# Optimization experiments

Measured on AMD Instinct MI355X. Metric: run time of the kernel, lower is better.

## Reference

```python
import jax, jax.numpy as jnp
import numpy as np

B, S, I, F = 2048, 512, 256, 256  # batch, seq_length, input_size, filter_num


def setup_inputs() -> dict:
    key = jax.random.key(0)
    ks = jax.random.split(key, 9)
    sc = 0.05
    return {
        "hidden": jax.random.normal(ks[0], (B, I), jnp.float32),
        "inp": jax.random.normal(ks[1], (B, S, I), jnp.float32),
        "W1": jax.random.normal(ks[2], (F, I), jnp.float32) * sc,   # linear1 weight (no bias)
        "Wc": jax.random.normal(ks[3], (F, S), jnp.float32) * sc,   # conv kernel [F,1,S,1] squeezed
        "bc": jax.random.normal(ks[4], (F,), jnp.float32) * sc,     # conv bias
        "W2": jax.random.normal(ks[5], (I, I + F), jnp.float32) * sc,
        "b2": jax.random.normal(ks[6], (I,), jnp.float32) * sc,
        "Wfc": jax.random.normal(ks[7], (1, I), jnp.float32) * sc,
        "bfc": jax.random.normal(ks[8], (1,), jnp.float32) * sc,
    }


def reference(hidden, inp, W1, Wc, bc, W2, b2, Wfc, bfc):
    # w = linear1(hidden).unsqueeze(1): [B,1,F]
    w = hidden @ W1.T  # [B,F]
    # Conv2d(1,F,kernel=(S,1)) over input [B,1,S,I] -> [B,F,1,I]; kernel spans full
    # time axis with width 1, so it's a contraction over t per input channel i.
    Hc_raw = jnp.einsum('bti,ft->bfi', inp, Wc) + bc[None, :, None]  # [B,F,I]
    # faithful to torch: .squeeze().reshape([-1, input_size, filter_num])
    H_c = Hc_raw.reshape(-1, I, F)  # [B,I,F]
    s = jnp.sum(H_c * w[:, None, :], axis=2)          # [B,I]
    a = jax.nn.sigmoid(s)
    v = jnp.sum(a[:, :, None] * H_c, axis=1)          # [B,F]
    concat = jnp.concatenate([hidden, v], axis=1)     # [B,I+F]
    h_prime = concat @ W2.T + b2                      # [B,I]
    out = h_prime @ Wfc.T + bfc                       # [B,1]
    return out
```

## Files before the change

kernel.cpp:

```cpp
#include <hip/hip_runtime.h>

#define B_ 2048
#define S_ 512
#define I_ 256
#define F_ 256
#define NG 8

#define OFF_W    0
#define OFF_SW   (OFF_W + B_*F_)
#define OFF_U    (OFF_SW + B_)
#define OFF_P    (OFF_U + B_*S_)
#define OFF_RP   (OFF_P + B_*S_)

__global__ __launch_bounds__(256) void k_pre(
    const float* __restrict__ hidden, const float* __restrict__ W1,
    const float* __restrict__ W2, const float* __restrict__ Wfc,
    float* __restrict__ ws) {
  const int tid = threadIdx.x;

  if (blockIdx.x >= B_ / 4) {
    const int g = blockIdx.x - B_ / 4;
    float acc0 = 0.f, acc1 = 0.f;
#pragma unroll 8
    for (int ii = 0; ii < 32; ++ii) {
      const int i = g * 32 + ii;
      const float f = Wfc[i];
      acc0 += f * W2[(size_t)i * (I_ + F_) + tid];
      acc1 += f * W2[(size_t)i * (I_ + F_) + tid + 256];
    }
    ws[OFF_RP + g * 512 + tid] = acc0;
    ws[OFF_RP + g * 512 + 256 + tid] = acc1;
    return;
  }

  __shared__ float h[4][I_];
  __shared__ float red[256];
  const int b0 = blockIdx.x * 4;
#pragma unroll
  for (int k = 0; k < 4; ++k) h[k][tid] = hidden[(size_t)(b0 + k) * I_ + tid];
  __syncthreads();

  const int f = tid;
  const float4* wrow = (const float4*)(W1 + (size_t)f * I_);
  float acc[4] = {0.f, 0.f, 0.f, 0.f};
#pragma unroll 4
  for (int iq = 0; iq < I_ / 4; ++iq) {
    const float4 v = wrow[iq];
    const int i = 4 * iq;
#pragma unroll
    for (int k = 0; k < 4; ++k)
      acc[k] += v.x * h[k][i] + v.y * h[k][i + 1] + v.z * h[k][i + 2] + v.w * h[k][i + 3];
  }
#pragma unroll
  for (int k = 0; k < 4; ++k) ws[OFF_W + (size_t)(b0 + k) * F_ + f] = acc[k];

#pragma unroll
  for (int k = 0; k < 4; ++k) {
    red[tid] = acc[k];
    __syncthreads();
    for (int s = 128; s > 0; s >>= 1) { if (tid < s) red[tid] += red[tid + s]; __syncthreads(); }
    if (tid == 0) ws[OFF_SW + b0 + k] = red[0];
    __syncthreads();
  }
}

__device__ __forceinline__ void dpp_sum64_dual(float& xu, float& xp) {
  int iu = __builtin_bit_cast(int, xu);
  int ip = __builtin_bit_cast(int, xp);
#define DPP_STEP(ctrl)                                                         \
  {                                                                            \
    int tu = __builtin_amdgcn_update_dpp(0, iu, (ctrl), 0xf, 0xf, true);       \
    int tp = __builtin_amdgcn_update_dpp(0, ip, (ctrl), 0xf, 0xf, true);       \
    iu = __builtin_bit_cast(int, __builtin_bit_cast(float, iu) +               \
                                     __builtin_bit_cast(float, tu));           \
    ip = __builtin_bit_cast(int, __builtin_bit_cast(float, ip) +               \
                                     __builtin_bit_cast(float, tp));           \
  }
  DPP_STEP(0x111)
  DPP_STEP(0x112)
  DPP_STEP(0x114)
  DPP_STEP(0x118)
  DPP_STEP(0x142)
  DPP_STEP(0x143)
#undef DPP_STEP
  xu = __builtin_bit_cast(float, iu);
  xp = __builtin_bit_cast(float, ip);
}

__global__ __launch_bounds__(256) void k1_scan(
    const float* __restrict__ inp, const float* __restrict__ wsw,
    const float* __restrict__ wsrp,
    float* __restrict__ wsu, float* __restrict__ wsp) {
  const int ROWS = 32;
  const int b = blockIdx.y;
  const int t0 = blockIdx.x * ROWS;
  const int tid = threadIdx.x;
  const int lane = tid & 63;
  const int wid = tid >> 6;

  __shared__ float rv_lds[F_];
  float rv = 0.f;
#pragma unroll
  for (int g = 0; g < NG; ++g) rv += wsrp[g * 512 + 256 + tid];
  rv_lds[tid] = rv;
  __syncthreads();

  const float4 w4  = ((const float4*)(wsw + (size_t)b * F_))[lane];
  const float4 rv4 = ((const float4*)rv_lds)[lane];
  const float* base = inp + ((size_t)b * S_ + t0) * I_;
  float* uo = wsu + (size_t)b * S_ + t0;
  float* po = wsp + (size_t)b * S_ + t0;

#pragma unroll
  for (int rr = 0; rr < ROWS / 4; ++rr) {
    const int row = wid + 4 * rr;
    const float4 in4 = ((const float4*)(base + (size_t)row * I_))[lane];
    float du = in4.x * w4.x + in4.y * w4.y + in4.z * w4.z + in4.w * w4.w;
    float dp = in4.x * rv4.x + in4.y * rv4.y + in4.z * rv4.z + in4.w * rv4.w;
    dpp_sum64_dual(du, dp);
    if (lane == 63) { uo[row] = du; po[row] = dp; }
  }
}

__global__ __launch_bounds__(256) void k2_epilogue(
    const float* __restrict__ Wc, const float* __restrict__ bc,
    const float* __restrict__ b2, const float* __restrict__ Wfc,
    const float* __restrict__ bfc, const float* __restrict__ hidden,
    const float* __restrict__ wsu, const float* __restrict__ wsp,
    const float* __restrict__ wsSw, const float* __restrict__ wsrp,
    float* __restrict__ out) {
  const int b0 = blockIdx.x * 4;
  const int tid = threadIdx.x;
  const int lane = tid & 63;
  const int wid = tid >> 6;
  __shared__ float u[4][S_];
  __shared__ float p[4][S_];
  __shared__ float redA[4], redB[4];
  __shared__ float wred[4][4];

  float rh = 0.f, rv = 0.f;
#pragma unroll
  for (int g = 0; g < NG; ++g) {
    rh += wsrp[g * 512 + tid];
    rv += wsrp[g * 512 + 256 + tid];
  }
  float t0 = rv, t1 = Wfc[tid] * b2[tid];
#pragma unroll
  for (int m = 32; m >= 1; m >>= 1) {
    t0 += __shfl_xor(t0, m, 64);
    t1 += __shfl_xor(t1, m, 64);
  }
  if (lane == 0) { redA[wid] = t0; redB[wid] = t1; }

#pragma unroll
  for (int k = 0; k < 4; ++k) {
    u[k][tid]       = wsu[(size_t)(b0 + k) * S_ + tid];
    u[k][tid + 256] = wsu[(size_t)(b0 + k) * S_ + tid + 256];
    p[k][tid]       = wsp[(size_t)(b0 + k) * S_ + tid];
    p[k][tid + 256] = wsp[(size_t)(b0 + k) * S_ + tid + 256];
  }
  __syncthreads();

  const float R  = redA[0] + redA[1] + redA[2] + redA[3];
  const float c0 = redB[0] + redB[1] + redB[2] + redB[3] + bfc[0];

  const int x = tid;
  const float4* wrow = (const float4*)(Wc + (size_t)x * S_);
  float ss[4] = {0.f, 0.f, 0.f, 0.f};
  float qs[4] = {0.f, 0.f, 0.f, 0.f};
#pragma unroll 4
  for (int tq = 0; tq < S_ / 4; ++tq) {
    const float4 v = wrow[tq];
    const int t = 4 * tq;
#pragma unroll
    for (int k = 0; k < 4; ++k) {
      ss[k] += v.x * u[k][t] + v.y * u[k][t + 1] + v.z * u[k][t + 2] + v.w * u[k][t + 3];
      qs[k] += v.x * p[k][t] + v.y * p[k][t + 1] + v.z * p[k][t + 2] + v.w * p[k][t + 3];
    }
  }

  const float bcx = bc[x];
#pragma unroll
  for (int k = 0; k < 4; ++k) {
    const float Sw = wsSw[b0 + k];
    const float s = ss[k] + bcx * Sw;
    const float a = 1.f / (1.f + expf(-s));
    float partial = a * (qs[k] + bcx * R) + rh * hidden[(size_t)(b0 + k) * I_ + x];
#pragma unroll
    for (int m = 32; m >= 1; m >>= 1) partial += __shfl_xor(partial, m, 64);
    if (lane == 0) wred[k][wid] = partial;
  }
  __syncthreads();
  if (tid < 4)
    out[b0 + tid] = wred[tid][0] + wred[tid][1] + wred[tid][2] + wred[tid][3] + c0;
}

extern "C" void kernel_launch(void* const* d_in, const int* in_sizes, int n_in,
                              void* d_out, int out_size, void* d_ws, size_t ws_size,
                              hipStream_t stream) {
  (void)in_sizes; (void)n_in; (void)out_size; (void)ws_size;
  const float* hidden = (const float*)d_in[0];
  const float* inp    = (const float*)d_in[1];
  const float* W1     = (const float*)d_in[2];
  const float* Wc     = (const float*)d_in[3];
  const float* bc     = (const float*)d_in[4];
  const float* W2     = (const float*)d_in[5];
  const float* b2     = (const float*)d_in[6];
  const float* Wfc    = (const float*)d_in[7];
  const float* bfc    = (const float*)d_in[8];
  float* out = (float*)d_out;
  float* ws  = (float*)d_ws;

  hipLaunchKernelGGL(k_pre, dim3(B_ / 4 + NG), dim3(256), 0, stream,
                     hidden, W1, W2, Wfc, ws);
  hipLaunchKernelGGL(k1_scan, dim3(S_ / 32, B_), dim3(256), 0, stream,
                     inp, ws + OFF_W, ws + OFF_RP, ws + OFF_U, ws + OFF_P);
  hipLaunchKernelGGL(k2_epilogue, dim3(B_ / 4), dim3(256), 0, stream,
                     Wc, bc, b2, Wfc, bfc, hidden,
                     ws + OFF_U, ws + OFF_P, ws + OFF_SW, ws + OFF_RP, out);
}
```

Measured before the change: 266.3 us.

## Fuse conv contraction into scan kernel with transposed Wc and chunked partials

Transposes Wc in the pre-kernel and adds a tiny mid kernel that precomputes the rh/rv vectors and scalar constants. The scan kernel now also contracts its chunk of u/p against the transposed Wc and writes per-chunk partial sums, so the epilogue only sums NCH partials per batch row instead of running a 512-long dot product from LDS. It picks the 8- or 4-chunk variant depending on workspace size, with the old path kept as fallback. This adds an extra launch and larger partial-sum writes, and makes each scan block re-read a slice of Wc.

Measured after the change: 264.2 us. About the same (-0.8%).

```diff
diff --git a/kernel.cpp b/kernel.cpp
--- a/kernel.cpp
+++ b/kernel.cpp
@@ -8,15 +8,41 @@
 
 #define OFF_W    0
 #define OFF_SW   (OFF_W + B_*F_)
-#define OFF_U    (OFF_SW + B_)
-#define OFF_P    (OFF_U + B_*S_)
-#define OFF_RP   (OFF_P + B_*S_)
+#define OFF_RP   (OFF_SW + B_)
+#define OFF_RH   (OFF_RP + NG*512)
+#define OFF_RV   (OFF_RH + 256)
+#define OFF_SC   (OFF_RV + 256)
+#define OFF_WCT  531456
+#define OFF_PS   (OFF_WCT + S_*F_)
+#define OFF_U2   OFF_WCT
+#define OFF_P2   (OFF_U2 + B_*S_)
 
 __global__ __launch_bounds__(256) void k_pre(
     const float* __restrict__ hidden, const float* __restrict__ W1,
     const float* __restrict__ W2, const float* __restrict__ Wfc,
-    float* __restrict__ ws) {
-  const int tid = threadIdx.x;
+    const float* __restrict__ Wc, float* __restrict__ ws) {
+  const int tid = threadIdx.x;
+
+  if (blockIdx.x >= B_ / 4 + NG) {
+    __shared__ float tile[64][65];
+    const int tt = blockIdx.x - (B_ / 4 + NG);
+    const int x0 = (tt & 3) * 64;
+    const int t0 = (tt >> 2) * 64;
+    const int col = tid & 63;
+    const int wid = tid >> 6;
+#pragma unroll
+    for (int r = 0; r < 16; ++r) {
+      const int row = r * 4 + wid;
+      tile[row][col] = Wc[(size_t)(x0 + row) * S_ + t0 + col];
+    }
+    __syncthreads();
+#pragma unroll
+    for (int r = 0; r < 16; ++r) {
+      const int trow = r * 4 + wid;
+      ws[OFF_WCT + (size_t)(t0 + trow) * F_ + x0 + col] = tile[col][trow];
+    }
+    return;
+  }
 
   if (blockIdx.x >= B_ / 4) {
     const int g = blockIdx.x - B_ / 4;
@@ -61,6 +87,37 @@
     for (int s = 128; s > 0; s >>= 1) { if (tid < s) red[tid] += red[tid + s]; __syncthreads(); }
     if (tid == 0) ws[OFF_SW + b0 + k] = red[0];
     __syncthreads();
+  }
+}
+
+__global__ __launch_bounds__(256) void k_mid(
+    const float* __restrict__ Wfc, const float* __restrict__ b2,
+    const float* __restrict__ bfc, float* __restrict__ ws) {
+  const int tid = threadIdx.x;
+  const int lane = tid & 63;
+  const int wid = tid >> 6;
+  __shared__ float redA[4], redB[4];
+
+  float rh = 0.f, rv = 0.f;
+#pragma unroll
+  for (int g = 0; g < NG; ++g) {
+    rh += ws[OFF_RP + g * 512 + tid];
+    rv += ws[OFF_RP + g * 512 + 256 + tid];
+  }
+  ws[OFF_RH + tid] = rh;
+  ws[OFF_RV + tid] = rv;
+
+  float t0 = rv, t1 = Wfc[tid] * b2[tid];
+#pragma unroll
+  for (int m = 32; m >= 1; m >>= 1) {
+    t0 += __shfl_xor(t0, m, 64);
+    t1 += __shfl_xor(t1, m, 64);
+  }
+  if (lane == 0) { redA[wid] = t0; redB[wid] = t1; }
+  __syncthreads();
+  if (tid == 0) {
+    ws[OFF_SC + 0] = redA[0] + redA[1] + redA[2] + redA[3];
+    ws[OFF_SC + 1] = redB[0] + redB[1] + redB[2] + redB[3] + bfc[0];
   }
 }
 
@@ -76,15 +133,91 @@
     ip = __builtin_bit_cast(int, __builtin_bit_cast(float, ip) +               \
                                      __builtin_bit_cast(float, tp));           \
   }
-  DPP_STEP(0x111)
-  DPP_STEP(0x112)
-  DPP_STEP(0x114)
-  DPP_STEP(0x118)
-  DPP_STEP(0x142)
-  DPP_STEP(0x143)
+  DPP_STEP(0x111) DPP_STEP(0x112) DPP_STEP(0x114) DPP_STEP(0x118)
+  DPP_STEP(0x142) DPP_STEP(0x143)
 #undef DPP_STEP
   xu = __builtin_bit_cast(float, iu);
   xp = __builtin_bit_cast(float, ip);
+}
+
+template <int NCH>
+__global__ __launch_bounds__(256) void k1_fused(
+    const float* __restrict__ inp, const float* __restrict__ wsw,
+    const float* __restrict__ wsrv, const float* __restrict__ wct,
+    float* __restrict__ ps, float* __restrict__ pq) {
+  constexpr int ROWS = S_ / NCH;
+  const int b = blockIdx.y;
+  const int cx = blockIdx.x;
+  const int t0 = cx * ROWS;
+  const int tid = threadIdx.x;
+  const int lane = tid & 63;
+  const int wid = tid >> 6;
+
+  __shared__ __align__(16) float u_l[ROWS];
+  __shared__ __align__(16) float p_l[ROWS];
+
+  const float4 w4  = ((const float4*)(wsw + (size_t)b * F_))[lane];
+  const float4 rv4 = ((const float4*)wsrv)[lane];
+  const float* base = inp + ((size_t)b * S_ + t0) * I_;
+
+#pragma unroll 4
+  for (int rr = 0; rr < ROWS / 4; ++rr) {
+    const int row = rr * 4 + wid;
+    const float4 in4 = ((const float4*)(base + (size_t)row * I_))[lane];
+    float du = in4.x * w4.x + in4.y * w4.y + in4.z * w4.z + in4.w * w4.w;
+    float dp = in4.x * rv4.x + in4.y * rv4.y + in4.z * rv4.z + in4.w * rv4.w;
+    dpp_sum64_dual(du, dp);
+    if (lane == 63) { u_l[row] = du; p_l[row] = dp; }
+  }
+  __syncthreads();
+
+  const float* wcol = wct + t0 * F_ + tid;
+  float ss = 0.f, qq = 0.f;
+#pragma unroll 4
+  for (int jq = 0; jq < ROWS / 4; ++jq) {
+    const float4 u4 = *(const float4*)&u_l[jq * 4];
+    const float4 p4 = *(const float4*)&p_l[jq * 4];
+    const float w0 = wcol[(size_t)(jq * 4 + 0) * F_];
+    const float w1 = wcol[(size_t)(jq * 4 + 1) * F_];
+    const float w2 = wcol[(size_t)(jq * 4 + 2) * F_];
+    const float w3 = wcol[(size_t)(jq * 4 + 3) * F_];
+    ss += w0 * u4.x + w1 * u4.y + w2 * u4.z + w3 * u4.w;
+    qq += w0 * p4.x + w1 * p4.y + w2 * p4.z + w3 * p4.w;
+  }
+  ps[((size_t)b * NCH + cx) * F_ + tid] = ss;
+  pq[((size_t)b * NCH + cx) * F_ + tid] = qq;
+}
+
+template <int NCH>
+__global__ __launch_bounds__(256) void k2_fused(
+    const float* __restrict__ bc, const float* __restrict__ hidden,
+    const float* __restrict__ wsSw, const float* __restrict__ wsrh,
+    const float* __restrict__ wssc,
+    const float* __restrict__ ps, const float* __restrict__ pq,
+    float* __restrict__ out) {
+  const int b = blockIdx.x;
+  const int x = threadIdx.x;
+  const int lane = x & 63;
+  const int wid = x >> 6;
+  __shared__ float red[4];
+
+  float s = 0.f, q = 0.f;
+#pragma unroll
+  for (int cx = 0; cx < NCH; ++cx) {
+    s += ps[((size_t)b * NCH + cx) * F_ + x];
+    q += pq[((size_t)b * NCH + cx) * F_ + x];
+  }
+  const float R  = wssc[0];
+  const float c0 = wssc[1];
+  const float bcx = bc[x];
+  s += bcx * wsSw[b];
+  const float a = 1.f / (1.f + expf(-s));
+  float partial = a * (q + bcx * R) + wsrh[x] * hidden[(size_t)b * I_ + x];
+#pragma unroll
+  for (int m = 32; m >= 1; m >>= 1) partial += __shfl_xor(partial, m, 64);
+  if (lane == 0) red[wid] = partial;
+  __syncthreads();
+  if (x == 0) out[b] = red[0] + red[1] + red[2] + red[3] + c0;
 }
 
 __global__ __launch_bounds__(256) void k1_scan(
@@ -117,8 +250,12 @@
     const float4 in4 = ((const float4*)(base + (size_t)row * I_))[lane];
     float du = in4.x * w4.x + in4.y * w4.y + in4.z * w4.z + in4.w * w4.w;
     float dp = in4.x * rv4.x + in4.y * rv4.y + in4.z * rv4.z + in4.w * rv4.w;
-    dpp_sum64_dual(du, dp);
-    if (lane == 63) { uo[row] = du; po[row] = dp; }
+#pragma unroll
+    for (int m = 32; m >= 1; m >>= 1) {
+      du += __shfl_xor(du, m, 64);
+      dp += __shfl_xor(dp, m, 64);
+    }
+    if (lane == 0) { uo[row] = du; po[row] = dp; }
   }
 }
 
@@ -198,7 +335,7 @@
 extern "C" void kernel_launch(void* const* d_in, const int* in_sizes, int n_in,
                               void* d_out, int out_size, void* d_ws, size_t ws_size,
                               hipStream_t stream) {
-  (void)in_sizes; (void)n_in; (void)out_size; (void)ws_size;
+  (void)in_sizes; (void)n_in; (void)out_size;
   const float* hidden = (const float*)d_in[0];
   const float* inp    = (const float*)d_in[1];
   const float* W1     = (const float*)d_in[2];
@@ -211,11 +348,32 @@
   float* out = (float*)d_out;
   float* ws  = (float*)d_ws;
 
-  hipLaunchKernelGGL(k_pre, dim3(B_ / 4 + NG), dim3(256), 0, stream,
-                     hidden, W1, W2, Wfc, ws);
-  hipLaunchKernelGGL(k1_scan, dim3(S_ / 32, B_), dim3(256), 0, stream,
-                     inp, ws + OFF_W, ws + OFF_RP, ws + OFF_U, ws + OFF_P);
-  hipLaunchKernelGGL(k2_epilogue, dim3(B_ / 4), dim3(256), 0, stream,
-                     Wc, bc, b2, Wfc, bfc, hidden,
-                     ws + OFF_U, ws + OFF_P, ws + OFF_SW, ws + OFF_RP, out);
-}
+  hipLaunchKernelGGL(k_pre, dim3(B_ / 4 + NG + 32), dim3(256), 0, stream,
+                     hidden, W1, W2, Wfc, Wc, ws);
+  hipLaunchKernelGGL(k_mid, dim3(1), dim3(256), 0, stream, Wfc, b2, bfc, ws);
+
+  const size_t need8 = ((size_t)OFF_PS + 2ull * B_ * 8 * F_) * 4;
+  const size_t need4 = ((size_t)OFF_PS + 2ull * B_ * 4 * F_) * 4;
+
+  if (ws_size >= need8) {
+    float* ps = ws + OFF_PS;
+    float* pq = ps + (size_t)B_ * 8 * F_;
+    hipLaunchKernelGGL(HIP_KERNEL_NAME(k1_fused<8>), dim3(8, B_), dim3(256), 0, stream,
+                       inp, ws + OFF_W, ws + OFF_RV, ws + OFF_WCT, ps, pq);
+    hipLaunchKernelGGL(HIP_KERNEL_NAME(k2_fused<8>), dim3(B_), dim3(256), 0, stream,
+                       bc, hidden, ws + OFF_SW, ws + OFF_RH, ws + OFF_SC, ps, pq, out);
+  } else if (ws_size >= need4) {
+    float* ps = ws + OFF_PS;
+    float* pq = ps + (size_t)B_ * 4 * F_;
+    hipLaunchKernelGGL(HIP_KERNEL_NAME(k1_fused<4>), dim3(4, B_), dim3(256), 0, stream,
+                       inp, ws + OFF_W, ws + OFF_RV, ws + OFF_WCT, ps, pq);
+    hipLaunchKernelGGL(HIP_KERNEL_NAME(k2_fused<4>), dim3(B_), dim3(256), 0, stream,
+                       bc, hidden, ws + OFF_SW, ws + OFF_RH, ws + OFF_SC, ps, pq, out);
+  } else {
+    hipLaunchKernelGGL(k1_scan, dim3(S_ / 32, B_), dim3(256), 0, stream,
+                       inp, ws + OFF_W, ws + OFF_RP, ws + OFF_U2, ws + OFF_P2);
+    hipLaunchKernelGGL(k2_epilogue, dim3(B_ / 4), dim3(256), 0, stream,
+                       Wc, bc, b2, Wfc, bfc, hidden,
+                       ws + OFF_U2, ws + OFF_P2, ws + OFF_SW, ws + OFF_RP, out);
+  }
+}
```
